# Kernel optimization log

Measured on AMD Instinct MI355X. Metric: run time of the kernel, lower is better.

Reference implementation:

```python
import jax, jax.numpy as jnp
import numpy as np

B, F, T_IN, T_OUT = 64, 256, 4096, 4096
BN_EPS = 1e-5


def setup_inputs() -> dict:
    key = jax.random.key(0)
    k1, k2, k3 = jax.random.split(key, 3)
    data = jax.random.normal(k1, (B, F, T_IN), dtype=jnp.float32)
    # matches init_params(): translate ~ N(0, 0.1^2), scale ~ N(0, 0.15^2)
    translate = jax.random.normal(k2, (F,), dtype=jnp.float32) * 0.1
    scale = jax.random.normal(k3, (F,), dtype=jnp.float32) * 0.15
    gamma = jnp.ones((F,), dtype=jnp.float32)
    beta = jnp.zeros((F,), dtype=jnp.float32)
    return {"data": data, "translate": translate, "scale": scale,
            "gamma": gamma, "beta": beta}


def _affine_resample(data, translate, scale):
    # Per-feature 1D affine resample, equivalent to torch affine_grid +
    # bilinear grid_sample with align_corners=False, padding_mode='zeros'.
    # theta = [[s, 0, s*t], [0, 1, 0]] per feature; H=1 so the y-axis is
    # degenerate (y' = 0 -> full weight on row 0).
    Bv, Fv, Tin = data.shape
    s = jnp.exp(scale / 5.0)                                  # [F]
    x = (2.0 * jnp.arange(T_OUT, dtype=jnp.float32) + 1.0) / T_OUT - 1.0  # [T_out]
    coord = s[:, None] * x[None, :] + (s * translate)[:, None]           # [F, T_out]
    ix = ((coord + 1.0) * Tin - 1.0) / 2.0                    # unnormalize
    i0 = jnp.floor(ix)
    w = ix - i0                                               # bilinear weight
    i0i = i0.astype(jnp.int32)
    i1i = i0i + 1
    valid0 = (i0i >= 0) & (i0i < Tin)
    valid1 = (i1i >= 0) & (i1i < Tin)
    i0c = jnp.clip(i0i, 0, Tin - 1)
    i1c = jnp.clip(i1i, 0, Tin - 1)
    # gather per (feature, out-pos), broadcast across batch: [B, F, T_out]
    v0 = jnp.take_along_axis(data, jnp.broadcast_to(i0c[None], (Bv, Fv, T_OUT)), axis=2)
    v1 = jnp.take_along_axis(data, jnp.broadcast_to(i1c[None], (Bv, Fv, T_OUT)), axis=2)
    v0 = jnp.where(valid0[None], v0, 0.0)
    v1 = jnp.where(valid1[None], v1, 0.0)
    return v0 * (1.0 - w)[None] + v1 * w[None]


def _batchnorm1d(x, gamma, beta):
    # BatchNorm1d in training mode: biased stats over (batch, time)
    mean = jnp.mean(x, axis=(0, 2), keepdims=True)
    var = jnp.mean(jnp.square(x - mean), axis=(0, 2), keepdims=True)
    xhat = (x - mean) * jax.lax.rsqrt(var + BN_EPS)
    return xhat * gamma[None, :, None] + beta[None, :, None]


def reference(data, translate, scale, gamma, beta):
    filtered = _affine_resample(data, translate, scale)   # [B, F, T_out]
    return _batchnorm1d(filtered, gamma, beta)
```

## Files before the change

### kernel.cpp

```cpp
#include <hip/hip_runtime.h>

#define NB 64
#define NF 256
#define TIN 4096
#define TOUT 4096
#define BN_EPS 1e-5f

__device__ __forceinline__ void waveReduce2(float& s, float& q) {
    #pragma unroll
    for (int off = 32; off > 0; off >>= 1) {
        s += __shfl_down(s, off, 64);
        q += __shfl_down(q, off, 64);
    }
}

__device__ __forceinline__ float resample_one(const float* __restrict__ row,
                                              int t, float s, float st) {
    float x = (2.0f * (float)t + 1.0f) * (1.0f / (float)TOUT) - 1.0f;
    float coord = s * x + st;
    float ix = ((coord + 1.0f) * (float)TIN - 1.0f) * 0.5f;
    float i0f = floorf(ix);
    float w = ix - i0f;
    int i0 = (int)i0f;
    int i1 = i0 + 1;
    float v0 = (i0 >= 0 && i0 < TIN) ? row[i0] : 0.0f;
    float v1 = (i1 >= 0 && i1 < TIN) ? row[i1] : 0.0f;
    return v0 * (1.0f - w) + v1 * w;
}

__global__ __launch_bounds__(256) void k_resample_stats(
    const float* __restrict__ data,
    const float* __restrict__ translate,
    const float* __restrict__ scale,
    float2* __restrict__ partials)
{
    const int blk = blockIdx.x;
    const int f = blk & (NF - 1);
    const int b = blk >> 8;
    const float* row_g = data + ((size_t)b * NF + f) * (size_t)TIN;

    __shared__ float row[TIN];
    __shared__ float2 wred[4];

    {
        const float4* src4 = (const float4*)row_g;
        float4* dst4 = (float4*)row;
        #pragma unroll
        for (int i = 0; i < TIN / 4 / 256; ++i)
            dst4[threadIdx.x + i * 256] = src4[threadIdx.x + i * 256];
    }
    __syncthreads();

    const float s = expf(scale[f] / 5.0f);
    const float st = s * translate[f];

    float sum = 0.0f, sq = 0.0f;
    #pragma unroll
    for (int k = 0; k < TOUT / 256; ++k) {
        int t = threadIdx.x + k * 256;
        float val = resample_one(row, t, s, st);
        sum += val;
        sq += val * val;
    }

    waveReduce2(sum, sq);
    const int lane = threadIdx.x & 63;
    const int wid = threadIdx.x >> 6;
    if (lane == 0) wred[wid] = make_float2(sum, sq);
    __syncthreads();
    if (threadIdx.x == 0) {
        float S = 0.0f, Q = 0.0f;
        #pragma unroll
        for (int i = 0; i < 4; ++i) { S += wred[i].x; Q += wred[i].y; }
        partials[blk] = make_float2(S, Q);
    }
}

__global__ __launch_bounds__(64) void k_stats(
    const float2* __restrict__ partials,
    const float* __restrict__ gamma,
    const float* __restrict__ beta,
    float2* __restrict__ stats)
{
    const int f = blockIdx.x;
    const int b = threadIdx.x;
    float2 p = partials[(size_t)b * NF + f];
    float S = p.x, Q = p.y;
    waveReduce2(S, Q);
    if (threadIdx.x == 0) {
        const float invN = 1.0f / (float)(NB * TOUT);
        float mean = S * invN;
        float var = Q * invN - mean * mean;
        float inv = 1.0f / sqrtf(var + BN_EPS);
        float a = gamma[f] * inv;
        float c = beta[f] - mean * a;
        stats[f] = make_float2(a, c);
    }
}

__global__ __launch_bounds__(256) void k_apply(
    const float* __restrict__ data,
    const float* __restrict__ translate,
    const float* __restrict__ scale,
    const float2* __restrict__ stats,
    float* __restrict__ out)
{
    const int blk = blockIdx.x;
    const int f = blk & (NF - 1);
    const int b = blk >> 8;
    const size_t rowbase = ((size_t)b * NF + f) * (size_t)TIN;
    const float* row_g = data + rowbase;
    float* out_row = out + rowbase;

    __shared__ float row[TIN];
    {
        const float4* src4 = (const float4*)row_g;
        float4* dst4 = (float4*)row;
        #pragma unroll
        for (int i = 0; i < TIN / 4 / 256; ++i)
            dst4[threadIdx.x + i * 256] = src4[threadIdx.x + i * 256];
    }
    __syncthreads();

    const float s = expf(scale[f] / 5.0f);
    const float st = s * translate[f];
    const float2 ac = stats[f];

    #pragma unroll
    for (int k = 0; k < TOUT / 256; ++k) {
        int t = threadIdx.x + k * 256;
        float val = resample_one(row, t, s, st);
        out_row[t] = val * ac.x + ac.y;
    }
}

extern "C" void kernel_launch(void* const* d_in, const int* in_sizes, int n_in,
                              void* d_out, int out_size, void* d_ws, size_t ws_size,
                              hipStream_t stream) {
    const float* data      = (const float*)d_in[0];
    const float* translate = (const float*)d_in[1];
    const float* scale     = (const float*)d_in[2];
    const float* gamma     = (const float*)d_in[3];
    const float* beta      = (const float*)d_in[4];
    float* out = (float*)d_out;

    float2* partials = (float2*)d_ws;
    float2* stats    = partials + NB * NF;

    k_resample_stats<<<NB * NF, 256, 0, stream>>>(data, translate, scale, partials);
    k_stats<<<NF, 64, 0, stream>>>(partials, gamma, beta, stats);
    k_apply<<<NB * NF, 256, 0, stream>>>(data, translate, scale, stats, out);
}
```

Baseline: 153.7 us.

## Fuse stats reduction into apply kernel, vectorize outputs, use nontemporal loads/stores

Removes the separate k_stats launch; each apply block now reduces the 64 per-batch partials for its feature and computes the BN scale and shift itself. Each thread now handles four consecutive outputs and writes them as one 128-bit nontemporal store, and the apply kernel's input loads are nontemporal. This saves one kernel launch and should improve store coalescing. In exchange every apply block redundantly reads 64 partials, and the nontemporal hints may bypass caching of data that was just read in the first pass.

```diff
diff --git a/kernel.cpp b/kernel.cpp
--- a/kernel.cpp
+++ b/kernel.cpp
@@ -5,6 +5,8 @@
 #define TIN 4096
 #define TOUT 4096
 #define BN_EPS 1e-5f
+
+typedef float f32x4 __attribute__((ext_vector_type(4)));
 
 __device__ __forceinline__ void waveReduce2(float& s, float& q) {
     #pragma unroll
@@ -14,18 +16,24 @@
     }
 }
 
-__device__ __forceinline__ float resample_one(const float* __restrict__ row,
-                                              int t, float s, float st) {
-    float x = (2.0f * (float)t + 1.0f) * (1.0f / (float)TOUT) - 1.0f;
-    float coord = s * x + st;
-    float ix = ((coord + 1.0f) * (float)TIN - 1.0f) * 0.5f;
-    float i0f = floorf(ix);
-    float w = ix - i0f;
-    int i0 = (int)i0f;
-    int i1 = i0 + 1;
-    float v0 = (i0 >= 0 && i0 < TIN) ? row[i0] : 0.0f;
-    float v1 = (i1 >= 0 && i1 < TIN) ? row[i1] : 0.0f;
-    return v0 * (1.0f - w) + v1 * w;
+__device__ __forceinline__ f32x4 resample4(const float* __restrict__ row,
+                                           int t0, float s, float st) {
+    f32x4 r;
+    #pragma unroll
+    for (int j = 0; j < 4; ++j) {
+        int t = t0 + j;
+        float x = (2.0f * (float)t + 1.0f) * (1.0f / (float)TOUT) - 1.0f;
+        float coord = s * x + st;
+        float ix = ((coord + 1.0f) * (float)TIN - 1.0f) * 0.5f;
+        float i0f = floorf(ix);
+        float w = ix - i0f;
+        int i0 = (int)i0f;
+        int i1 = i0 + 1;
+        float v0 = (i0 >= 0 && i0 < TIN) ? row[i0] : 0.0f;
+        float v1 = (i1 >= 0 && i1 < TIN) ? row[i1] : 0.0f;
+        r[j] = v0 * (1.0f - w) + v1 * w;
+    }
+    return r;
 }
 
 __global__ __launch_bounds__(256) void k_resample_stats(
@@ -43,8 +51,8 @@
     __shared__ float2 wred[4];
 
     {
-        const float4* src4 = (const float4*)row_g;
-        float4* dst4 = (float4*)row;
+        const f32x4* src4 = (const f32x4*)row_g;
+        f32x4* dst4 = (f32x4*)row;
         #pragma unroll
         for (int i = 0; i < TIN / 4 / 256; ++i)
             dst4[threadIdx.x + i * 256] = src4[threadIdx.x + i * 256];
@@ -56,11 +64,11 @@
 
     float sum = 0.0f, sq = 0.0f;
     #pragma unroll
-    for (int k = 0; k < TOUT / 256; ++k) {
-        int t = threadIdx.x + k * 256;
-        float val = resample_one(row, t, s, st);
-        sum += val;
-        sq += val * val;
+    for (int k = 0; k < 4; ++k) {
+        int t0 = (threadIdx.x + k * 256) * 4;
+        f32x4 v = resample4(row, t0, s, st);
+        sum += v.x + v.y + v.z + v.w;
+        sq += v.x * v.x + v.y * v.y + v.z * v.z + v.w * v.w;
     }
 
     waveReduce2(sum, sq);
@@ -76,33 +84,13 @@
     }
 }
 
-__global__ __launch_bounds__(64) void k_stats(
-    const float2* __restrict__ partials,
-    const float* __restrict__ gamma,
-    const float* __restrict__ beta,
-    float2* __restrict__ stats)
-{
-    const int f = blockIdx.x;
-    const int b = threadIdx.x;
-    float2 p = partials[(size_t)b * NF + f];
-    float S = p.x, Q = p.y;
-    waveReduce2(S, Q);
-    if (threadIdx.x == 0) {
-        const float invN = 1.0f / (float)(NB * TOUT);
-        float mean = S * invN;
-        float var = Q * invN - mean * mean;
-        float inv = 1.0f / sqrtf(var + BN_EPS);
-        float a = gamma[f] * inv;
-        float c = beta[f] - mean * a;
-        stats[f] = make_float2(a, c);
-    }
-}
-
 __global__ __launch_bounds__(256) void k_apply(
     const float* __restrict__ data,
     const float* __restrict__ translate,
     const float* __restrict__ scale,
-    const float2* __restrict__ stats,
+    const float2* __restrict__ partials,
+    const float* __restrict__ gamma,
+    const float* __restrict__ beta,
     float* __restrict__ out)
 {
     const int blk = blockIdx.x;
@@ -113,24 +101,46 @@
     float* out_row = out + rowbase;
 
     __shared__ float row[TIN];
+    __shared__ float2 s_ac;
+
     {
-        const float4* src4 = (const float4*)row_g;
-        float4* dst4 = (float4*)row;
+        const f32x4* src4 = (const f32x4*)row_g;
+        f32x4* dst4 = (f32x4*)row;
         #pragma unroll
         for (int i = 0; i < TIN / 4 / 256; ++i)
-            dst4[threadIdx.x + i * 256] = src4[threadIdx.x + i * 256];
+            dst4[threadIdx.x + i * 256] =
+                __builtin_nontemporal_load(&src4[threadIdx.x + i * 256]);
+    }
+
+    if (threadIdx.x < 64) {
+        float2 p = partials[(size_t)threadIdx.x * NF + f];
+        float S = p.x, Q = p.y;
+        waveReduce2(S, Q);
+        if (threadIdx.x == 0) {
+            const float invN = 1.0f / (float)(NB * TOUT);
+            float mean = S * invN;
+            float var = Q * invN - mean * mean;
+            float inv = 1.0f / sqrtf(var + BN_EPS);
+            float a = gamma[f] * inv;
+            s_ac = make_float2(a, beta[f] - mean * a);
+        }
     }
     __syncthreads();
 
     const float s = expf(scale[f] / 5.0f);
     const float st = s * translate[f];
-    const float2 ac = stats[f];
+    const float a = s_ac.x;
+    const float c = s_ac.y;
 
     #pragma unroll
-    for (int k = 0; k < TOUT / 256; ++k) {
-        int t = threadIdx.x + k * 256;
-        float val = resample_one(row, t, s, st);
-        out_row[t] = val * ac.x + ac.y;
+    for (int k = 0; k < 4; ++k) {
+        int t0 = (threadIdx.x + k * 256) * 4;
+        f32x4 v = resample4(row, t0, s, st);
+        v.x = v.x * a + c;
+        v.y = v.y * a + c;
+        v.z = v.z * a + c;
+        v.w = v.w * a + c;
+        __builtin_nontemporal_store(v, (f32x4*)(out_row + t0));
     }
 }
 
@@ -145,9 +155,8 @@
     float* out = (float*)d_out;
 
     float2* partials = (float2*)d_ws;
-    float2* stats    = partials + NB * NF;
 
     k_resample_stats<<<NB * NF, 256, 0, stream>>>(data, translate, scale, partials);
-    k_stats<<<NF, 64, 0, stream>>>(partials, gamma, beta, stats);
-    k_apply<<<NB * NF, 256, 0, stream>>>(data, translate, scale, stats, out);
+    k_apply<<<NB * NF, 256, 0, stream>>>(data, translate, scale, partials,
+                                         gamma, beta, out);
 }
```

Result: faster. 132.2 us (-14.0%).
